# Optimization experiments

Hardware: AMD Instinct MI355X
Metric: run time of the kernel (lower is better)

The kernel has to match this reference:

```python
import jax, jax.numpy as jnp
import numpy as np

B = 4
N_CPGS = 20000
N_FREQS = N_CPGS // 2 + 1  # rfft length
E = 320000
H = 4
HD = 16          # head_dim = graph_hidden // n_heads
GH = 64          # graph_hidden
FD = 64          # fusion_dim
FH = 128         # fft_hidden
PH = 128         # plasticity_hidden


def _ln(x, g, b, eps=1e-5):
    m = x.mean(-1, keepdims=True)
    v = ((x - m) ** 2).mean(-1, keepdims=True)
    return (x - m) / jnp.sqrt(v + eps) * g + b


def _gelu(x):
    return jax.nn.gelu(x, approximate=False)  # torch default: exact erf GELU


def setup_inputs() -> dict:
    key = jax.random.key(0)
    ki = iter(jax.random.split(key, 40))
    nrm = lambda shape, s=0.02: jax.random.normal(next(ki), shape, dtype=jnp.float32) * s
    z = lambda *s: jnp.zeros(s, jnp.float32)
    o = lambda *s: jnp.ones(s, jnp.float32)
    return dict(
        x=jax.random.uniform(next(ki), (B, N_CPGS), dtype=jnp.float32),
        edge_index=jax.random.randint(next(ki), (2, E), 0, N_CPGS, dtype=jnp.int32),
        fft_freq_weights=o(N_FREQS),
        fft_w1=nrm((FH, N_FREQS)), fft_b1=z(FH), fft_ln1_g=o(FH), fft_ln1_b=z(FH),
        fft_w2=nrm((FD, FH)), fft_b2=z(FD), fft_ln2_g=o(FD), fft_ln2_b=z(FD),
        ge_w=nrm((GH, 1)), ge_b=z(GH), ge_ln_g=o(GH), ge_ln_b=z(GH),
        gat_w=nrm((GH, GH)), gat_attn=nrm((H, 2 * HD), 0.1),
        gp_w=nrm((FD, GH)), gp_b=z(FD), gp_ln_g=o(FD), gp_ln_b=z(FD),
        pl_W=nrm((PH, N_FREQS), 0.01), pl_alpha=o(PH, N_FREQS) * 0.01,
        pl_eta=jnp.array([0.1], jnp.float32), pl_bias=z(PH),
        pn_g=o(PH), pn_b=z(PH),
        pp_w=nrm((FD, PH)), pp_b=z(FD), pp_ln_g=o(FD), pp_ln_b=z(FD),
        gate_w1=nrm((6, 3 * FD)), gate_b1=z(6), gate_w2=nrm((3, 6)), gate_b2=z(3),
        head_w1=nrm((32, FD)), head_b1=z(32), head_w2=nrm((1, 32)), head_b2=z(1),
    )


def reference(x, edge_index, fft_freq_weights,
              fft_w1, fft_b1, fft_ln1_g, fft_ln1_b, fft_w2, fft_b2, fft_ln2_g, fft_ln2_b,
              ge_w, ge_b, ge_ln_g, ge_ln_b, gat_w, gat_attn,
              gp_w, gp_b, gp_ln_g, gp_ln_b,
              pl_W, pl_alpha, pl_eta, pl_bias, pn_g, pn_b,
              pp_w, pp_b, pp_ln_g, pp_ln_b,
              gate_w1, gate_b1, gate_w2, gate_b2,
              head_w1, head_b1, head_w2, head_b2):
    Bsz, n = x.shape
    # ---- Stream 1: FFT ----
    xc = x - x.mean(axis=1, keepdims=True)
    mag = jnp.log1p(jnp.abs(jnp.fft.rfft(xc, axis=1)))          # (B, N_FREQS)
    freq_w = jax.nn.softmax(fft_freq_weights) * fft_freq_weights.shape[0]
    magw = mag * freq_w[None, :]
    f = _gelu(_ln(magw @ fft_w1.T + fft_b1, fft_ln1_g, fft_ln1_b))
    fft_feat = _ln(f @ fft_w2.T + fft_b2, fft_ln2_g, fft_ln2_b)  # (B, FD)
    # ---- Stream 2: sparse graph attention (eval: dropout off) ----
    h0 = _gelu(_ln(x[..., None] * ge_w[:, 0] + ge_b, ge_ln_g, ge_ln_b))  # (B, N, GH)
    h = (h0 @ gat_w.T).reshape(Bsz, n, H, HD)
    a_src, a_dst = gat_attn[:, :HD], gat_attn[:, HD:]
    s_src = jnp.einsum('bnhd,hd->bnh', h, a_src)
    s_dst = jnp.einsum('bnhd,hd->bnh', h, a_dst)
    src, dst = edge_index[0], edge_index[1]
    scores = s_src[:, src] + s_dst[:, dst]                       # (B, E, H)
    scores = jnp.where(scores >= 0, scores, 0.2 * scores)        # leaky_relu(0.2)
    # max with include_self=True over zero-init buffer (matches torch scatter_reduce)
    m = jnp.zeros((Bsz, n, H), scores.dtype).at[:, dst].max(scores)
    e = jnp.exp(scores - m[:, dst])
    ssum = jnp.zeros((Bsz, n, H), e.dtype).at[:, dst].add(e)
    attn = e / (ssum[:, dst] + 1e-8)
    msg = h[:, src] * attn[..., None]                            # (B, E, H, HD)
    gat_out = jnp.zeros((Bsz, n, H, HD), msg.dtype).at[:, dst].add(msg).reshape(Bsz, n, H * HD)
    hg = h0 + _gelu(gat_out)
    graph_feat = _ln(hg.mean(axis=1) @ gp_w.T + gp_b, gp_ln_g, gp_ln_b)  # (B, FD)
    # ---- Stream 3: Hebbian plastic layer on mag ----
    y_slow = mag @ pl_W.T + pl_bias                              # (B, PH)
    x_norm = mag / (jnp.linalg.norm(mag, axis=-1, keepdims=True) + 1e-8)
    y_pre = jnp.tanh(y_slow)
    # bmm(alpha * eta * outer(y_pre, x_norm), x) == eta * y_pre * ((x_norm*x) @ alpha.T)
    contrib = pl_eta[0] * y_pre * ((x_norm * mag) @ jax.nn.sigmoid(pl_alpha).T)
    plastic = _ln(_gelu(y_slow + contrib), pn_g, pn_b)
    plastic_feat = _ln(plastic @ pp_w.T + pp_b, pp_ln_g, pp_ln_b)
    # ---- Gated fusion ----
    concat = jnp.concatenate([fft_feat, graph_feat, plastic_feat], axis=-1)  # (B, 3*FD)
    g = _gelu(concat @ gate_w1.T + gate_b1) @ gate_w2.T + gate_b2
    gw = jax.nn.softmax(g, axis=-1)                              # (B, 3)
    fused = fft_feat * gw[:, 0:1] + graph_feat * gw[:, 1:2] + plastic_feat * gw[:, 2:3]
    # ---- Head ----
    out = _gelu(fused @ head_w1.T + head_b1) @ head_w2.T + head_b2
    return out.squeeze(-1)                                       # (B,)
```

## Files before the change

kernel.cpp:

```cpp
#include <hip/hip_runtime.h>
#include <math.h>

constexpr int N_CPGS = 20000;
constexpr int NF     = 10001;
constexpr int BZ     = 4;
constexpr int NEDGE  = 320000;
constexpr int KPAD   = 10240;
constexpr int FN1    = 200;
constexpr int FN2    = 100;
constexpr int TILES  = (N_CPGS + 63) / 64;
constexpr int HB     = NEDGE / 256;
constexpr int DOTSB  = 384;
constexpr int GATB   = 4096;

constexpr size_t W_XMEAN   = 0;
constexpr size_t W_SMSTAT  = 64;
constexpr size_t W_NORMSQ  = 128;
constexpr size_t W_H0SUM   = 192;
constexpr size_t W_GATMEAN = 448;
constexpr size_t W_PREP    = 704;
constexpr size_t W_D       = 768;
constexpr size_t W_MAG     = 2304;
constexpr size_t W_SSRC    = 42368;
constexpr size_t W_SDST    = 362368;
constexpr size_t W_H       = 682368;
constexpr size_t W_Y       = 5802368;
constexpr size_t W_COUNTS  = 9079168;
constexpr size_t W_OFFS    = 9099168;
constexpr size_t W_CURSOR  = 9119232;
constexpr size_t W_SORTSRC = 9139232;

#define DEVFN static __device__ __forceinline__

DEVFN float gelu_f(float v) {
    float ax = fabsf(v) * 0.70710678118654752440f;
    float t = 1.0f / fmaf(0.3275911f, ax, 1.0f);
    float p = fmaf(t, 1.061405429f, -1.453152027f);
    p = fmaf(p, t, 1.421413741f);
    p = fmaf(p, t, -0.284496736f);
    p = fmaf(p, t, 0.254829592f);
    p = p * t;
    float e = __expf(-ax * ax);
    float er = copysignf(fmaf(-p, e, 1.0f), v);
    return 0.5f * v * (1.0f + er);
}

DEVFN float wred_sum(float v) {
    #pragma unroll
    for (int m = 32; m; m >>= 1) v += __shfl_xor(v, m);
    return v;
}

DEVFN unsigned int bfr(float f) {
    unsigned int u = __float_as_uint(f);
    return (u + 0x7fffu + ((u >> 16) & 1u)) >> 16;
}
DEVFN float bf2f(unsigned short v) { return __uint_as_float(((unsigned int)v) << 16); }

__global__ void k_pre(const float* __restrict__ x, const float* __restrict__ ge_w,
                      const float* __restrict__ ge_b, const float* __restrict__ fw,
                      const int* __restrict__ ei, float* __restrict__ ws) {
    int bb = blockIdx.x, t = threadIdx.x;
    __shared__ float sd[256];
    if (bb >= 26) {
        int e = (bb - 26) * 256 + t;
        if (e < NEDGE) atomicAdd((int*)(ws + W_COUNTS) + ei[NEDGE + e], 1);
        return;
    }
    if (bb < 4) {
        const float4* x4 = (const float4*)(x + (size_t)bb * N_CPGS);
        float s = 0.f;
        for (int i = t; i < N_CPGS / 4; i += 256) {
            float4 v = x4[i];
            s += (v.x + v.y) + (v.z + v.w);
        }
        sd[t] = s; __syncthreads();
        for (int o = 128; o; o >>= 1) { if (t < o) sd[t] += sd[t + o]; __syncthreads(); }
        if (t == 0) ws[W_XMEAN + bb] = sd[0] * (1.0f / N_CPGS);
    } else if (bb == 4) {
        for (int i = t; i < (int)(W_PREP - W_NORMSQ); i += 256) ws[W_NORMSQ + i] = 0.f;
        if (t < 64) {
            float w = ge_w[t], b = ge_b[t];
            float mw = wred_sum(w) * (1.f / 64.f);
            float mb = wred_sum(b) * (1.f / 64.f);
            float wc = w - mw, bc = b - mb;
            float A = wred_sum(wc * wc) * (1.f / 64.f);
            float C = wred_sum(wc * bc) * (1.f / 64.f);
            float D = wred_sum(bc * bc) * (1.f / 64.f);
            if (t == 0) { float* p = ws + W_PREP; p[0] = mw; p[1] = mb; p[2] = A; p[3] = C; p[4] = D; }
        }
    } else if (bb == 5) {
        float mx = -1e30f;
        for (int i = t; i < NF; i += 256) mx = fmaxf(mx, fw[i]);
        sd[t] = mx; __syncthreads();
        for (int o = 128; o; o >>= 1) { if (t < o) sd[t] = fmaxf(sd[t], sd[t + o]); __syncthreads(); }
        mx = sd[0]; __syncthreads();
        float s = 0.f;
        for (int i = t; i < NF; i += 256) s += expf(fw[i] - mx);
        sd[t] = s; __syncthreads();
        for (int o = 128; o; o >>= 1) { if (t < o) sd[t] += sd[t + o]; __syncthreads(); }
        if (t == 0) { ws[W_SMSTAT] = mx; ws[W_SMSTAT + 1] = sd[0]; }
    }
}

__global__ __launch_bounds__(256) void k_node(
    const float* __restrict__ x, const float* __restrict__ ge_w, const float* __restrict__ ge_b,
    const float* __restrict__ ge_g, const float* __restrict__ ge_beta,
    const float* __restrict__ gat_w, const float* __restrict__ gat_attn,
    float* __restrict__ ws)
{
    int t = threadIdx.x;
    int nb = blockIdx.x;
    if (nb == 0) {
        const int* cnt = (const int*)(ws + W_COUNTS);
        int* offs = (int*)(ws + W_OFFS);
        int* cur  = (int*)(ws + W_CURSOR);
        constexpr int PER = (N_CPGS + 255) / 256;
        int i0 = t * PER;
        int s = 0;
        for (int i = 0; i < PER; ++i) { int idx = i0 + i; if (idx < N_CPGS) s += cnt[idx]; }
        __shared__ int sdi[256];
        sdi[t] = s; __syncthreads();
        for (int off = 1; off < 256; off <<= 1) {
            int v = (t >= off) ? sdi[t - off] : 0;
            __syncthreads();
            sdi[t] += v;
            __syncthreads();
        }
        int run = sdi[t] - s;
        for (int i = 0; i < PER; ++i) {
            int idx = i0 + i;
            if (idx < N_CPGS) { offs[idx] = run; cur[idx] = run; run += cnt[idx]; }
        }
        if (t == 255) offs[N_CPGS] = sdi[255];
        return;
    }
    if (nb >= 1 + 4 * TILES) {
        int fb = nb - 1 - 4 * TILES;
        int b = fb / 100;
        int n1base = (fb % 100) * 2;
        int n1l = t >> 7, k2 = t & 127;
        __shared__ float xs[2][100];
        float xm = ws[W_XMEAN + b];
        for (int i = t; i < 200; i += 256) {
            int nl = (i >= 100) ? 1 : 0, n2 = (i >= 100) ? i - 100 : i;
            xs[nl][n2] = x[(size_t)b * N_CPGS + n1base + nl + 200 * n2] - xm;
        }
        __syncthreads();
        int k2e = (k2 < 100) ? k2 : 0;
        constexpr float T100 = 6.2831853071795864769f / 100.f;
        float dc, dsn;
        { float sn, cn; sincosf(T100 * (float)k2e, &sn, &cn); dc = cn; dsn = -sn; }
        float yr = 0.f, yi = 0.f;
        #pragma unroll
        for (int half = 0; half < 2; ++half) {
            float c, s;
            { int m = (k2e * (half * 50)) % 100; float sn, cn; sincosf(T100 * (float)m, &sn, &cn); c = cn; s = -sn; }
            #pragma unroll 5
            for (int j = 0; j < 50; ++j) {
                float xv = xs[n1l][half * 50 + j];
                yr = fmaf(xv, c, yr); yi = fmaf(xv, s, yi);
                float tc_ = c * dc - s * dsn; s = s * dc + c * dsn; c = tc_;
            }
        }
        if (k2 < 100)
            ((float2*)(ws + W_Y))[((size_t)(n1base + n1l) * FN2 + k2) * 4 + b] = make_float2(yr, yi);
        return;
    }
    int nb2 = nb - 1;
    int b = nb2 / TILES;
    int tile = nb2 % TILES;
    int n0 = tile * 64;

    __shared__ __align__(16) float h0T[64 * 68];
    __shared__ __align__(16) float gwT[64 * 68];
    __shared__ float xsv[64], rss[64];

    const float* prep = ws + W_PREP;
    float mw = prep[0], mb = prep[1], A = prep[2], C = prep[3], Dd = prep[4];

    for (int idx = t; idx < 4096; idx += 256) { int i = idx >> 6, j = idx & 63; gwT[j * 68 + i] = gat_w[idx]; }
    if (t < 64) {
        int n = n0 + t;
        float xv = (n < N_CPGS) ? x[(size_t)b * N_CPGS + n] : 0.f;
        xsv[t] = xv;
        float var = xv * xv * A + 2.f * xv * C + Dd;
        rss[t] = 1.0f / sqrtf(var + 1e-5f);
    }
    __syncthreads();

    for (int idx = t; idx < 4096; idx += 256) {
        int j = idx >> 6, nd = idx & 63;
        float h0 = 0.f;
        if (n0 + nd < N_CPGS) {
            float v = (xsv[nd] * (ge_w[j] - mw) + (ge_b[j] - mb)) * rss[nd];
            h0 = gelu_f(v * ge_g[j] + ge_beta[j]);
        }
        h0T[j * 68 + nd] = h0;
    }
    __syncthreads();

    int tr = t >> 4, tc = t & 15;
    float acc[4][4] = {};
    #pragma unroll 8
    for (int j = 0; j < 64; ++j) {
        const float4 av = *(const float4*)&h0T[j * 68 + (tr << 2)];
        const float4 bv = *(const float4*)&gwT[j * 68 + (tc << 2)];
        #pragma unroll
        for (int u = 0; u < 4; ++u) {
            float a = (u == 0) ? av.x : (u == 1) ? av.y : (u == 2) ? av.z : av.w;
            acc[u][0] = fmaf(a, bv.x, acc[u][0]);
            acc[u][1] = fmaf(a, bv.y, acc[u][1]);
            acc[u][2] = fmaf(a, bv.z, acc[u][2]);
            acc[u][3] = fmaf(a, bv.w, acc[u][3]);
        }
    }
    if (t < 64) {
        float s = 0.f;
        #pragma unroll 8
        for (int nd = 0; nd < 64; ++nd) s += h0T[t * 68 + nd];
        atomicAdd(ws + W_H0SUM + b * 64 + t, s);
    }
    unsigned short* hbp = (unsigned short*)(ws + W_H);
    #pragma unroll
    for (int u = 0; u < 4; ++u) {
        int n = n0 + tr * 4 + u;
        if (n < N_CPGS) {
            unsigned int lo = bfr(acc[u][0]) | (bfr(acc[u][1]) << 16);
            unsigned int hi = bfr(acc[u][2]) | (bfr(acc[u][3]) << 16);
            *(uint2*)(hbp + ((size_t)b * N_CPGS + n) * 64 + tc * 4) = make_uint2(lo, hi);
        }
    }
    {
        int hh = tc >> 2;
        float ps[4], pd[4];
        #pragma unroll
        for (int u = 0; u < 4; ++u) {
            float s = 0.f, d = 0.f;
            #pragma unroll
            for (int kk = 0; kk < 4; ++kk) {
                float asv = gat_attn[hh * 32 + (tc & 3) * 4 + kk];
                float adv = gat_attn[hh * 32 + 16 + (tc & 3) * 4 + kk];
                s = fmaf(acc[u][kk], asv, s);
                d = fmaf(acc[u][kk], adv, d);
            }
            ps[u] = s; pd[u] = d;
        }
        #pragma unroll
        for (int u = 0; u < 4; ++u) {
            ps[u] += __shfl_xor(ps[u], 1); ps[u] += __shfl_xor(ps[u], 2);
            pd[u] += __shfl_xor(pd[u], 1); pd[u] += __shfl_xor(pd[u], 2);
        }
        if ((tc & 3) == 0) {
            #pragma unroll
            for (int u = 0; u < 4; ++u) {
                int n = n0 + tr * 4 + u;
                if (n < N_CPGS) {
                    ws[W_SSRC + ((size_t)b * N_CPGS + n) * 4 + hh] = ps[u];
                    ws[W_SDST + ((size_t)b * N_CPGS + n) * 4 + hh] = pd[u];
                }
            }
        }
    }
}

__global__ __launch_bounds__(256) void k_scat2(const int* __restrict__ ei,
                                               float* __restrict__ ws) {
    int t = threadIdx.x;
    if (blockIdx.x < HB) {
        int e = blockIdx.x * 256 + t;
        if (e < NEDGE) {
            int s = ei[e], d = ei[NEDGE + e];
            int pos = atomicAdd((int*)(ws + W_CURSOR) + d, 1);
            ((int*)(ws + W_SORTSRC))[pos] = s;
        }
        return;
    }
    int gid = (blockIdx.x - HB) * 256 + t;
    int k = gid >> 2, b = gid & 3;
    int k2 = k % 100;
    const float2* Y2 = (const float2*)(ws + W_Y);
    constexpr float W0 = 6.2831853071795864769f / 20000.f;
    float dc, dsn;
    { float sn, cn; sincosf(W0 * (float)k, &sn, &cn); dc = cn; dsn = -sn; }
    float xr = 0.f, xi = 0.f;
    #pragma unroll
    for (int seg = 0; seg < 4; ++seg) {
        int n1b = seg * 50;
        float c, s;
        { int m = (k * n1b) % 20000; float sn, cn; sincosf(W0 * (float)m, &sn, &cn); c = cn; s = -sn; }
        #pragma unroll 5
        for (int j = 0; j < 50; ++j) {
            float2 y = Y2[((size_t)(n1b + j) * FN2 + k2) * 4 + b];
            xr = fmaf(y.x, c, xr); xr = fmaf(-y.y, s, xr);
            xi = fmaf(y.x, s, xi); xi = fmaf( y.y, c, xi);
            float tc_ = c * dc - s * dsn; s = s * dc + c * dsn; c = tc_;
        }
    }
    bool ok = k < NF;
    float m = 0.f;
    if (ok) {
        m = log1pf(sqrtf(xr * xr + xi * xi));
        ws[W_MAG + (size_t)b * NF + k] = m;
    }
    float msq = ok ? m * m : 0.f;
    #pragma unroll
    for (int o = 4; o < 64; o <<= 1) msq += __shfl_xor(msq, o);
    if ((t & 63) < 4) atomicAdd(ws + W_NORMSQ + b, msq);
}

__global__ __launch_bounds__(256) void k_gatdots(
    const float* __restrict__ fftw1, const float* __restrict__ plW,
    const float* __restrict__ plalpha, const float* __restrict__ fw,
    float* __restrict__ ws)
{
    int t = threadIdx.x;
    if (blockIdx.x >= DOTSB) {
        int g = blockIdx.x - DOTSB;
        int xcd = g & 7;
        int b = xcd >> 1;
        int blk = ((g >> 3) << 1) | (xcd & 1);
        int w = t >> 6, lane = t & 63;
        int wv = blk * 4 + w;
        int egrp = lane >> 4, fgrp = lane & 15;
        int hh = fgrp >> 2;
        const int* offs = (const int*)(ws + W_OFFS);
        const int* ssrt = (const int*)(ws + W_SORTSRC);
        const float4* s4src = (const float4*)(ws + W_SSRC);
        const float4* s4dst = (const float4*)(ws + W_SDST);
        const uint2* hbp = (const uint2*)(ws + W_H);
        size_t bN = (size_t)b * N_CPGS;
        float gacc0 = 0.f, gacc1 = 0.f, gacc2 = 0.f, gacc3 = 0.f;

        __shared__ float elds[4][4][68];
        __shared__ int   slds[4][68];
        __shared__ float gred[4][64];

        for (int dst = wv; dst < N_CPGS; dst += GATB) {
            int o0 = offs[dst], o1 = offs[dst + 1];
            if (o0 == o1) continue;
            float4 sd4 = s4dst[bN + dst];
            float es = 0.f;
            float a0 = 0.f, a1 = 0.f, a2 = 0.f, a3 = 0.f;
            for (int c0 = o0; c0 < o1; c0 += 64) {
                int cnt = min(64, o1 - c0);
                float v0 = 0.f, v1 = 0.f, v2 = 0.f, v3 = 0.f;
                int s = 0;
                if (lane < cnt) {
                    s = ssrt[c0 + lane];
                    float4 ss = s4src[bN + s];
                    v0 = ss.x + sd4.x; v0 = (v0 >= 0.f) ? v0 : 0.2f * v0; v0 = __expf(v0);
                    v1 = ss.y + sd4.y; v1 = (v1 >= 0.f) ? v1 : 0.2f * v1; v1 = __expf(v1);
                    v2 = ss.z + sd4.z; v2 = (v2 >= 0.f) ? v2 : 0.2f * v2; v2 = __expf(v2);
                    v3 = ss.w + sd4.w; v3 = (v3 >= 0.f) ? v3 : 0.2f * v3; v3 = __expf(v3);
                }
                slds[w][lane] = s;
                elds[w][0][lane] = v0; elds[w][1][lane] = v1;
                elds[w][2][lane] = v2; elds[w][3][lane] = v3;
                int niter = (cnt + 3) >> 2;
                for (int i = 0; i < niter; ++i) {
                    int j = (i << 2) + egrp;
                    float e = elds[w][hh][j];
                    int sj = slds[w][j];
                    uint2 hv = hbp[(bN + sj) * 16 + fgrp];
                    es += e;
                    a0 = fmaf(e, bf2f((unsigned short)(hv.x & 0xffffu)), a0);
                    a1 = fmaf(e, bf2f((unsigned short)(hv.x >> 16)),     a1);
                    a2 = fmaf(e, bf2f((unsigned short)(hv.y & 0xffffu)), a2);
                    a3 = fmaf(e, bf2f((unsigned short)(hv.y >> 16)),     a3);
                }
            }
            es += __shfl_xor(es, 16); es += __shfl_xor(es, 32);
            a0 += __shfl_xor(a0, 16); a0 += __shfl_xor(a0, 32);
            a1 += __shfl_xor(a1, 16); a1 += __shfl_xor(a1, 32);
            a2 += __shfl_xor(a2, 16); a2 += __shfl_xor(a2, 32);
            a3 += __shfl_xor(a3, 16); a3 += __shfl_xor(a3, 32);
            float inv = 1.f / (es + 1e-8f);
            gacc0 += gelu_f(a0 * inv); gacc1 += gelu_f(a1 * inv);
            gacc2 += gelu_f(a2 * inv); gacc3 += gelu_f(a3 * inv);
        }
        if (egrp == 0) {
            gred[w][fgrp * 4 + 0] = gacc0; gred[w][fgrp * 4 + 1] = gacc1;
            gred[w][fgrp * 4 + 2] = gacc2; gred[w][fgrp * 4 + 3] = gacc3;
        }
        __syncthreads();
        if (t < 64)
            atomicAdd(ws + W_GATMEAN + b * 64 + t, gred[0][t] + gred[1][t] + gred[2][t] + gred[3][t]);
        return;
    }
    int bb2 = blockIdx.x;
    int m = bb2 >> 7;
    int r = bb2 & 127;
    const float* mag = ws + W_MAG;
    float smx = ws[W_SMSTAT], ssm = ws[W_SMSTAT + 1];
    float sc_fw = (float)NF / ssm;
    float inv_n0 = 1.f / (sqrtf(ws[W_NORMSQ + 0]) + 1e-8f);
    float inv_n1 = 1.f / (sqrtf(ws[W_NORMSQ + 1]) + 1e-8f);
    float inv_n2 = 1.f / (sqrtf(ws[W_NORMSQ + 2]) + 1e-8f);
    float inv_n3 = 1.f / (sqrtf(ws[W_NORMSQ + 3]) + 1e-8f);
    const float* row = ((m == 0) ? fftw1 : (m == 1) ? plW : plalpha) + (size_t)r * NF;
    float a0 = 0.f, a1 = 0.f, a2 = 0.f, a3 = 0.f;
    for (int k = t; k < NF; k += 256) {
        float wv = row[k];
        float g0 = mag[k], g1 = mag[NF + k], g2 = mag[2 * NF + k], g3 = mag[3 * NF + k];
        if (m == 0) {
            float s = expf(fw[k] - smx) * sc_fw;
            wv *= s;
            a0 = fmaf(wv, g0, a0); a1 = fmaf(wv, g1, a1); a2 = fmaf(wv, g2, a2); a3 = fmaf(wv, g3, a3);
        } else if (m == 1) {
            a0 = fmaf(wv, g0, a0); a1 = fmaf(wv, g1, a1); a2 = fmaf(wv, g2, a2); a3 = fmaf(wv, g3, a3);
        } else {
            wv = 1.f / (1.f + expf(-wv));
            a0 = fmaf(wv, g0 * g0 * inv_n0, a0); a1 = fmaf(wv, g1 * g1 * inv_n1, a1);
            a2 = fmaf(wv, g2 * g2 * inv_n2, a2); a3 = fmaf(wv, g3 * g3 * inv_n3, a3);
        }
    }
    __shared__ float sd[256];
    float acc[4] = {a0, a1, a2, a3};
    #pragma unroll
    for (int bb = 0; bb < 4; ++bb) {
        sd[t] = acc[bb]; __syncthreads();
        for (int o = 128; o; o >>= 1) { if (t < o) sd[t] += sd[t + o]; __syncthreads(); }
        if (t == 0) ws[W_D + ((size_t)m * 128 + r) * 4 + bb] = sd[0];
        __syncthreads();
    }
}

DEVFN float ln64(float v, const float* g, const float* bt, int lane) {
    float mn = wred_sum(v) * (1.f / 64.f);
    float d = v - mn;
    float var = wred_sum(d * d) * (1.f / 64.f);
    return d * (1.0f / sqrtf(var + 1e-5f)) * g[lane] + bt[lane];
}
DEVFN void ln128(float& v0, float& v1, const float* g, const float* bt, int lane) {
    float mn = wred_sum(v0 + v1) * (1.f / 128.f);
    float d0 = v0 - mn, d1 = v1 - mn;
    float var = wred_sum(d0 * d0 + d1 * d1) * (1.f / 128.f);
    float rs = 1.0f / sqrtf(var + 1e-5f);
    v0 = d0 * rs * g[lane] + bt[lane];
    v1 = d1 * rs * g[lane + 64] + bt[lane + 64];
}
DEVFN float dotW128(const float* __restrict__ W, const float* __restrict__ v, int c) {
    const float4* w4 = (const float4*)(W + (size_t)c * 128);
    float acc = 0.f;
    #pragma unroll
    for (int q = 0; q < 32; ++q) {
        float4 wv = w4[q];
        const float* vv = v + q * 4;
        acc = fmaf(wv.x, vv[0], acc); acc = fmaf(wv.y, vv[1], acc);
        acc = fmaf(wv.z, vv[2], acc); acc = fmaf(wv.w, vv[3], acc);
    }
    return acc;
}
DEVFN float dotW64(const float* __restrict__ W, const float* __restrict__ v, int c) {
    const float4* w4 = (const float4*)(W + (size_t)c * 64);
    float acc = 0.f;
    #pragma unroll
    for (int q = 0; q < 16; ++q) {
        float4 wv = w4[q];
        const float* vv = v + q * 4;
        acc = fmaf(wv.x, vv[0], acc); acc = fmaf(wv.y, vv[1], acc);
        acc = fmaf(wv.z, vv[2], acc); acc = fmaf(wv.w, vv[3], acc);
    }
    return acc;
}

__global__ __launch_bounds__(256) void k_final(
    const float* __restrict__ fft_b1, const float* __restrict__ fft_ln1_g, const float* __restrict__ fft_ln1_b,
    const float* __restrict__ fft_w2, const float* __restrict__ fft_b2,
    const float* __restrict__ fft_ln2_g, const float* __restrict__ fft_ln2_b,
    const float* __restrict__ gp_w, const float* __restrict__ gp_b,
    const float* __restrict__ gp_ln_g, const float* __restrict__ gp_ln_b,
    const float* __restrict__ pl_eta, const float* __restrict__ pl_bias,
    const float* __restrict__ pn_g, const float* __restrict__ pn_b,
    const float* __restrict__ pp_w, const float* __restrict__ pp_b,
    const float* __restrict__ pp_ln_g, const float* __restrict__ pp_ln_b,
    const float* __restrict__ gate_w1, const float* __restrict__ gate_b1,
    const float* __restrict__ gate_w2, const float* __restrict__ gate_b2,
    const float* __restrict__ head_w1, const float* __restrict__ head_b1,
    const float* __restrict__ head_w2, const float* __restrict__ head_b2,
    float* __restrict__ ws, float* __restrict__ out)
{
    int t = threadIdx.x, b = t >> 6, lane = t & 63;
    __shared__ float vlds[4][256];
    float* vb = vlds[b];
    const float* D = ws + W_D;
    int r0 = lane, r1 = lane + 64;

    float f0 = D[(0 * 128 + r0) * 4 + b] + fft_b1[r0];
    float f1 = D[(0 * 128 + r1) * 4 + b] + fft_b1[r1];
    ln128(f0, f1, fft_ln1_g, fft_ln1_b, lane);
    vb[lane] = gelu_f(f0); vb[64 + lane] = gelu_f(f1);
    float catf = ln64(dotW128(fft_w2, vb, lane) + fft_b2[lane], fft_ln2_g, fft_ln2_b, lane);

    float hgm = (ws[W_H0SUM + b * 64 + lane] + ws[W_GATMEAN + b * 64 + lane]) * (1.f / N_CPGS);
    vb[lane] = hgm;
    float catg = ln64(dotW64(gp_w, vb, lane) + gp_b[lane], gp_ln_g, gp_ln_b, lane);

    float eta = pl_eta[0];
    float ys0 = D[(1 * 128 + r0) * 4 + b] + pl_bias[r0];
    float ys1 = D[(1 * 128 + r1) * 4 + b] + pl_bias[r1];
    float q0 = D[(2 * 128 + r0) * 4 + b];
    float q1 = D[(2 * 128 + r1) * 4 + b];
    float u0 = gelu_f(ys0 + eta * tanhf(ys0) * q0);
    float u1 = gelu_f(ys1 + eta * tanhf(ys1) * q1);
    ln128(u0, u1, pn_g, pn_b, lane);
    vb[lane] = u0; vb[64 + lane] = u1;
    float catp = ln64(dotW128(pp_w, vb, lane) + pp_b[lane], pp_ln_g, pp_ln_b, lane);

    vb[lane] = catf; vb[64 + lane] = catg; vb[128 + lane] = catp;
    if (lane < 6) {
        float a = gate_b1[lane];
        const float* wrow = gate_w1 + lane * 192;
        #pragma unroll 4
        for (int j = 0; j < 192; ++j) a = fmaf(wrow[j], vb[j], a);
        vb[192 + lane] = gelu_f(a);
    }
    float gv[3];
    #pragma unroll
    for (int c = 0; c < 3; ++c) {
        float a = gate_b2[c];
        #pragma unroll
        for (int j = 0; j < 6; ++j) a = fmaf(gate_w2[c * 6 + j], vb[192 + j], a);
        gv[c] = a;
    }
    float gmx = fmaxf(gv[0], fmaxf(gv[1], gv[2]));
    float e0 = expf(gv[0] - gmx), e1 = expf(gv[1] - gmx), e2 = expf(gv[2] - gmx);
    float inv = 1.f / (e0 + e1 + e2);
    float fus = catf * (e0 * inv) + catg * (e1 * inv) + catp * (e2 * inv);

    vb[lane] = fus;
    float hval = 0.f;
    if (lane < 32) {
        float a = dotW64(head_w1, vb, lane) + head_b1[lane];
        hval = gelu_f(a) * head_w2[lane];
    }
    float o = wred_sum(hval);
    if (lane == 0) out[b] = o + head_b2[0];
}

extern "C" void kernel_launch(void* const* d_in, const int* in_sizes, int n_in,
                              void* d_out, int out_size, void* d_ws, size_t ws_size,
                              hipStream_t stream) {
    (void)in_sizes; (void)n_in; (void)out_size; (void)ws_size;
    const float* x        = (const float*)d_in[0];
    const int*   ei       = (const int*)d_in[1];
    const float* fw       = (const float*)d_in[2];
    const float* fft_w1   = (const float*)d_in[3];
    const float* fft_b1   = (const float*)d_in[4];
    const float* fft_ln1g = (const float*)d_in[5];
    const float* fft_ln1b = (const float*)d_in[6];
    const float* fft_w2   = (const float*)d_in[7];
    const float* fft_b2   = (const float*)d_in[8];
    const float* fft_ln2g = (const float*)d_in[9];
    const float* fft_ln2b = (const float*)d_in[10];
    const float* ge_w     = (const float*)d_in[11];
    const float* ge_b     = (const float*)d_in[12];
    const float* ge_g     = (const float*)d_in[13];
    const float* ge_beta  = (const float*)d_in[14];
    const float* gat_w    = (const float*)d_in[15];
    const float* gat_attn = (const float*)d_in[16];
    const float* gp_w     = (const float*)d_in[17];
    const float* gp_b     = (const float*)d_in[18];
    const float* gp_ln_g  = (const float*)d_in[19];
    const float* gp_ln_b  = (const float*)d_in[20];
    const float* pl_W     = (const float*)d_in[21];
    const float* pl_alpha = (const float*)d_in[22];
    const float* pl_eta   = (const float*)d_in[23];
    const float* pl_bias  = (const float*)d_in[24];
    const float* pn_g     = (const float*)d_in[25];
    const float* pn_b     = (const float*)d_in[26];
    const float* pp_w     = (const float*)d_in[27];
    const float* pp_b     = (const float*)d_in[28];
    const float* pp_ln_g  = (const float*)d_in[29];
    const float* pp_ln_b  = (const float*)d_in[30];
    const float* gate_w1  = (const float*)d_in[31];
    const float* gate_b1  = (const float*)d_in[32];
    const float* gate_w2  = (const float*)d_in[33];
    const float* gate_b2  = (const float*)d_in[34];
    const float* head_w1  = (const float*)d_in[35];
    const float* head_b1  = (const float*)d_in[36];
    const float* head_w2  = (const float*)d_in[37];
    const float* head_b2  = (const float*)d_in[38];

    float* ws  = (float*)d_ws;
    float* out = (float*)d_out;

    hipMemsetAsync(ws + W_COUNTS, 0, N_CPGS * sizeof(int), stream);
    k_pre<<<26 + HB, 256, 0, stream>>>(x, ge_w, ge_b, fw, ei, ws);
    k_node<<<1 + 4 * TILES + 400, 256, 0, stream>>>(x, ge_w, ge_b, ge_g, ge_beta,
                                                    gat_w, gat_attn, ws);
    k_scat2<<<HB + 160, 256, 0, stream>>>(ei, ws);
    k_gatdots<<<DOTSB + GATB, 256, 0, stream>>>(fft_w1, pl_W, pl_alpha, fw, ws);
    k_final<<<1, 256, 0, stream>>>(fft_b1, fft_ln1g, fft_ln1b, fft_w2, fft_b2, fft_ln2g, fft_ln2b,
                                   gp_w, gp_b, gp_ln_g, gp_ln_b, pl_eta, pl_bias, pn_g, pn_b,
                                   pp_w, pp_b, pp_ln_g, pp_ln_b, gate_w1, gate_b1, gate_w2, gate_b2,
                                   head_w1, head_b1, head_w2, head_b2, ws, out);
}
```

Baseline: 203.1 us.

## Compute node embedding and GAT projection per-thread in registers instead of LDS tiles

Replaces the 64-node shared-memory tiled GEMM in the node stage with one node per thread, holding the 64-wide h0 vector in registers and reading gat_w rows as uniform (scalar/broadcast) loads. The h0 column sums are built with wavefront reductions, and the attention src/dst scores are written as float4. This removes LDS staging, the barriers, and the transpose of gat_w. In exchange it adds heavy register pressure from the 64-float array and lowers occupancy. The per-thread stores of bf16 rows are also strided, which weakens coalescing.

```diff
diff --git a/kernel.cpp b/kernel.cpp
--- a/kernel.cpp
+++ b/kernel.cpp
@@ -8,10 +8,11 @@
 constexpr int KPAD   = 10240;
 constexpr int FN1    = 200;
 constexpr int FN2    = 100;
-constexpr int TILES  = (N_CPGS + 63) / 64;
 constexpr int HB     = NEDGE / 256;
 constexpr int DOTSB  = 384;
 constexpr int GATB   = 4096;
+constexpr int BPB    = 79;
+constexpr int NODEB  = 4 * BPB;
 
 constexpr size_t W_XMEAN   = 0;
 constexpr size_t W_SMSTAT  = 64;
@@ -135,8 +136,8 @@
         if (t == 255) offs[N_CPGS] = sdi[255];
         return;
     }
-    if (nb >= 1 + 4 * TILES) {
-        int fb = nb - 1 - 4 * TILES;
+    if (nb >= 1 + NODEB) {
+        int fb = nb - 1 - NODEB;
         int b = fb / 100;
         int n1base = (fb % 100) * 2;
         int n1l = t >> 7, k2 = t & 127;
@@ -167,100 +168,78 @@
             ((float2*)(ws + W_Y))[((size_t)(n1base + n1l) * FN2 + k2) * 4 + b] = make_float2(yr, yi);
         return;
     }
-    int nb2 = nb - 1;
-    int b = nb2 / TILES;
-    int tile = nb2 % TILES;
-    int n0 = tile * 64;
-
-    __shared__ __align__(16) float h0T[64 * 68];
-    __shared__ __align__(16) float gwT[64 * 68];
-    __shared__ float xsv[64], rss[64];
+    int tile = nb - 1;
+    int b = tile / BPB;
+    int lt = tile - b * BPB;
+    int n = lt * 256 + t;
+    bool act = n < N_CPGS;
+    int lane = t & 63;
 
     const float* prep = ws + W_PREP;
     float mw = prep[0], mb = prep[1], A = prep[2], C = prep[3], Dd = prep[4];
 
-    for (int idx = t; idx < 4096; idx += 256) { int i = idx >> 6, j = idx & 63; gwT[j * 68 + i] = gat_w[idx]; }
-    if (t < 64) {
-        int n = n0 + t;
-        float xv = (n < N_CPGS) ? x[(size_t)b * N_CPGS + n] : 0.f;
-        xsv[t] = xv;
-        float var = xv * xv * A + 2.f * xv * C + Dd;
-        rss[t] = 1.0f / sqrtf(var + 1e-5f);
-    }
-    __syncthreads();
-
-    for (int idx = t; idx < 4096; idx += 256) {
-        int j = idx >> 6, nd = idx & 63;
-        float h0 = 0.f;
-        if (n0 + nd < N_CPGS) {
-            float v = (xsv[nd] * (ge_w[j] - mw) + (ge_b[j] - mb)) * rss[nd];
-            h0 = gelu_f(v * ge_g[j] + ge_beta[j]);
-        }
-        h0T[j * 68 + nd] = h0;
-    }
-    __syncthreads();
-
-    int tr = t >> 4, tc = t & 15;
-    float acc[4][4] = {};
-    #pragma unroll 8
+    float xv = act ? x[(size_t)b * N_CPGS + n] : 0.f;
+    float rs = 1.0f / sqrtf(fmaf(xv * A, xv, fmaf(2.f * C, xv, Dd)) + 1e-5f);
+    float axn = xv * rs;
+
+    float h0[64];
+    #pragma unroll
     for (int j = 0; j < 64; ++j) {
-        const float4 av = *(const float4*)&h0T[j * 68 + (tr << 2)];
-        const float4 bv = *(const float4*)&gwT[j * 68 + (tc << 2)];
+        float v = fmaf(fmaf(axn, ge_w[j] - mw, (ge_b[j] - mb) * rs), ge_g[j], ge_beta[j]);
+        h0[j] = act ? gelu_f(v) : 0.f;
+    }
+
+    {
+        float msum = 0.f;
         #pragma unroll
-        for (int u = 0; u < 4; ++u) {
-            float a = (u == 0) ? av.x : (u == 1) ? av.y : (u == 2) ? av.z : av.w;
-            acc[u][0] = fmaf(a, bv.x, acc[u][0]);
-            acc[u][1] = fmaf(a, bv.y, acc[u][1]);
-            acc[u][2] = fmaf(a, bv.z, acc[u][2]);
-            acc[u][3] = fmaf(a, bv.w, acc[u][3]);
-        }
-    }
-    if (t < 64) {
-        float s = 0.f;
-        #pragma unroll 8
-        for (int nd = 0; nd < 64; ++nd) s += h0T[t * 68 + nd];
-        atomicAdd(ws + W_H0SUM + b * 64 + t, s);
-    }
-    unsigned short* hbp = (unsigned short*)(ws + W_H);
-    #pragma unroll
-    for (int u = 0; u < 4; ++u) {
-        int n = n0 + tr * 4 + u;
-        if (n < N_CPGS) {
-            unsigned int lo = bfr(acc[u][0]) | (bfr(acc[u][1]) << 16);
-            unsigned int hi = bfr(acc[u][2]) | (bfr(acc[u][3]) << 16);
-            *(uint2*)(hbp + ((size_t)b * N_CPGS + n) * 64 + tc * 4) = make_uint2(lo, hi);
-        }
-    }
-    {
-        int hh = tc >> 2;
-        float ps[4], pd[4];
-        #pragma unroll
-        for (int u = 0; u < 4; ++u) {
-            float s = 0.f, d = 0.f;
+        for (int j = 0; j < 64; ++j) {
+            float s = wred_sum(h0[j]);
+            if (lane == j) msum = s;
+        }
+        atomicAdd(ws + W_H0SUM + b * 64 + lane, msum);
+    }
+
+    unsigned short* hrow = (unsigned short*)(ws + W_H) + ((size_t)b * N_CPGS + n) * 64;
+    float ss0 = 0.f, ss1 = 0.f, ss2 = 0.f, ss3 = 0.f;
+    float sD0 = 0.f, sD1 = 0.f, sD2 = 0.f, sD3 = 0.f;
+    #pragma unroll
+    for (int hh = 0; hh < 4; ++hh) {
+        float sacc = 0.f, dacc = 0.f;
+        for (int i4 = 0; i4 < 4; ++i4) {
+            int i0 = hh * 16 + i4 * 4;
+            const float* w0 = gat_w + (size_t)(i0 + 0) * 64;
+            const float* w1 = gat_w + (size_t)(i0 + 1) * 64;
+            const float* w2 = gat_w + (size_t)(i0 + 2) * 64;
+            const float* w3 = gat_w + (size_t)(i0 + 3) * 64;
+            float ac0 = 0.f, ac1 = 0.f, ac2 = 0.f, ac3 = 0.f;
             #pragma unroll
-            for (int kk = 0; kk < 4; ++kk) {
-                float asv = gat_attn[hh * 32 + (tc & 3) * 4 + kk];
-                float adv = gat_attn[hh * 32 + 16 + (tc & 3) * 4 + kk];
-                s = fmaf(acc[u][kk], asv, s);
-                d = fmaf(acc[u][kk], adv, d);
+            for (int j = 0; j < 64; ++j) {
+                float hv = h0[j];
+                ac0 = fmaf(hv, w0[j], ac0);
+                ac1 = fmaf(hv, w1[j], ac1);
+                ac2 = fmaf(hv, w2[j], ac2);
+                ac3 = fmaf(hv, w3[j], ac3);
             }
-            ps[u] = s; pd[u] = d;
-        }
-        #pragma unroll
-        for (int u = 0; u < 4; ++u) {
-            ps[u] += __shfl_xor(ps[u], 1); ps[u] += __shfl_xor(ps[u], 2);
-            pd[u] += __shfl_xor(pd[u], 1); pd[u] += __shfl_xor(pd[u], 2);
-        }
-        if ((tc & 3) == 0) {
-            #pragma unroll
-            for (int u = 0; u < 4; ++u) {
-                int n = n0 + tr * 4 + u;
-                if (n < N_CPGS) {
-                    ws[W_SSRC + ((size_t)b * N_CPGS + n) * 4 + hh] = ps[u];
-                    ws[W_SDST + ((size_t)b * N_CPGS + n) * 4 + hh] = pd[u];
-                }
+            const float* asrc = gat_attn + hh * 32 + i4 * 4;
+            sacc = fmaf(ac0, asrc[0], sacc); sacc = fmaf(ac1, asrc[1], sacc);
+            sacc = fmaf(ac2, asrc[2], sacc); sacc = fmaf(ac3, asrc[3], sacc);
+            dacc = fmaf(ac0, asrc[16], dacc); dacc = fmaf(ac1, asrc[17], dacc);
+            dacc = fmaf(ac2, asrc[18], dacc); dacc = fmaf(ac3, asrc[19], dacc);
+            if (act) {
+                uint2 pv;
+                pv.x = bfr(ac0) | (bfr(ac1) << 16);
+                pv.y = bfr(ac2) | (bfr(ac3) << 16);
+                *(uint2*)(hrow + i0) = pv;
             }
         }
+        if (hh == 0) { ss0 = sacc; sD0 = dacc; }
+        else if (hh == 1) { ss1 = sacc; sD1 = dacc; }
+        else if (hh == 2) { ss2 = sacc; sD2 = dacc; }
+        else { ss3 = sacc; sD3 = dacc; }
+    }
+    if (act) {
+        *(float4*)(ws + W_SSRC + ((size_t)b * N_CPGS + n) * 4) = make_float4(ss0, ss1, ss2, ss3);
+        *(float4*)(ws + W_SDST + ((size_t)b * N_CPGS + n) * 4) = make_float4(sD0, sD1, sD2, sD3);
     }
 }
 
@@ -588,8 +567,8 @@
 
     hipMemsetAsync(ws + W_COUNTS, 0, N_CPGS * sizeof(int), stream);
     k_pre<<<26 + HB, 256, 0, stream>>>(x, ge_w, ge_b, fw, ei, ws);
-    k_node<<<1 + 4 * TILES + 400, 256, 0, stream>>>(x, ge_w, ge_b, ge_g, ge_beta,
-                                                    gat_w, gat_attn, ws);
+    k_node<<<1 + NODEB + 400, 256, 0, stream>>>(x, ge_w, ge_b, ge_g, ge_beta,
+                                                gat_w, gat_attn, ws);
     k_scat2<<<HB + 160, 256, 0, stream>>>(ei, ws);
     k_gatdots<<<DOTSB + GATB, 256, 0, stream>>>(fft_w1, pl_W, pl_alpha, fw, ws);
     k_final<<<1, 256, 0, stream>>>(fft_b1, fft_ln1g, fft_ln1b, fft_w2, fft_b2, fft_ln2g, fft_ln2b,
```

After: 207.6 us. 2.2% more time.
